# Optimization experiments

Measured on AMD Instinct MI355X. Metric: run time of the kernel, lower is better.

The kernel has to match this reference:

```python
import jax, jax.numpy as jnp
import numpy as np

# ---- quantization constants (8-bit, per-tensor affine; representative values) ----
Q_MAX = 255.0
S_IN, Z_IN = 0.05, 128.0      # block input
S1, Z1 = 0.04, 128.0          # after expand 1x1 + hardswish
S2, Z2 = 0.04, 128.0          # after depthwise 5x5 + hardswish
S_SE1, Z_SE1 = 0.03, 128.0    # SE fc1 output
S_SE2, Z_SE2 = 1.0 / 255.0, 0.0  # SE fc2 hardsigmoid output in [0,1]
S_MUL, Z_MUL = 0.04, 128.0    # SE gated activation
S3, Z3 = 0.05, 128.0          # after project 1x1
S_OUT, Z_OUT = 0.06, 128.0    # after residual add
W_SCALE = 0.01                # symmetric per-tensor weight scale (zero_point = 0)
EXP_C = 576                   # expanded channels (depthwise groups)


def conv(x, w, stride=1, padding=0, groups=1):
    return jax.lax.conv_general_dilated(
        x, w, (stride, stride), [(padding, padding), (padding, padding)],
        feature_group_count=groups, dimension_numbers=('NCHW', 'OIHW', 'NCHW'))


def hardswish(x):
    return x * jnp.clip(x + 3.0, 0.0, 6.0) * (1.0 / 6.0)


def hardsigmoid(x):
    return jnp.clip(x + 3.0, 0.0, 6.0) * (1.0 / 6.0)


def qconv(x_q, w_q, b_q, s_in, z_in, s_out, z_out, stride=1, padding=0, groups=1, act=None):
    """Quantized conv: int-domain accumulation (simulated in fp32), fused activation
    on the dequantized accumulator, then requantize to [0, Q_MAX]."""
    acc = conv(x_q - z_in, w_q, stride, padding, groups) + b_q[None, :, None, None]
    deq = acc * (s_in * W_SCALE)  # dequantize accumulator
    if act == 'hardswish':
        deq = hardswish(deq)
    elif act == 'hardsigmoid':
        deq = hardsigmoid(deq)
    return jnp.clip(deq * (1.0 / s_out) + z_out, 0.0, Q_MAX)


def setup_inputs() -> dict:
    key = jax.random.key(0)
    ks = jax.random.split(key, 11)
    def qw(k, shape):  # int8-style symmetric weights stored as fp32 integers
        return jnp.round(jnp.clip(jax.random.normal(k, shape) * 40.0, -127.0, 127.0))
    def qb(k, n):      # int32-style bias in accumulator domain
        return jnp.round(jax.random.normal(k, (n,)) * 500.0)
    return {
        'x':      jnp.round(jax.random.uniform(ks[0], (64, 96, 28, 28)) * Q_MAX),
        'w_exp':  qw(ks[1], (576, 96, 1, 1)),  'b_exp':  qb(ks[2], 576),
        'w_dw':   qw(ks[3], (576, 1, 5, 5)),   'b_dw':   qb(ks[4], 576),
        'w_se1':  qw(ks[5], (144, 576, 1, 1)), 'b_se1':  qb(ks[6], 144),
        'w_se2':  qw(ks[7], (576, 144, 1, 1)), 'b_se2':  qb(ks[8], 576),
        'w_proj': qw(ks[9], (96, 576, 1, 1)),  'b_proj': qb(ks[10], 96),
    }


def reference(x, w_exp, b_exp, w_dw, b_dw, w_se1, b_se1, w_se2, b_se2, w_proj, b_proj):
    # expand 1x1 (+ hardswish)
    e = qconv(x, w_exp, b_exp, S_IN, Z_IN, S1, Z1, act='hardswish')
    # depthwise 5x5, padding=(5-1)//2=2, groups=expanded (+ hardswish)
    d = qconv(e, w_dw, b_dw, S1, Z1, S2, Z2, padding=2, groups=EXP_C, act='hardswish')
    # squeeze-excitation: global avg pool -> fc1 -> fc2(hardsigmoid) -> quantized mul
    pooled = jnp.mean(d, axis=(2, 3), keepdims=True)  # [N, 576, 1, 1]
    g1 = qconv(pooled, w_se1, b_se1, S2, Z2, S_SE1, Z_SE1)
    g2 = qconv(g1, w_se2, b_se2, S_SE1, Z_SE1, S_SE2, Z_SE2, act='hardsigmoid')
    gated = jnp.clip((g2 - Z_SE2) * (d - Z2) * (S_SE2 * S2 / S_MUL) + Z_MUL, 0.0, Q_MAX)
    # project 1x1 (linear)
    p = qconv(gated, w_proj, b_proj, S_MUL, Z_MUL, S3, Z3)
    # quantized residual add (stride=1, in==out channels -> use_res_connect)
    out = jnp.clip((x - Z_IN) * (S_IN / S_OUT) + (p - Z3) * (S3 / S_OUT) + Z_OUT, 0.0, Q_MAX)
    return out
```

## Files before the change

kernel.cpp:

```cpp
#include <hip/hip_runtime.h>

typedef _Float16 v8h __attribute__((ext_vector_type(8)));
typedef _Float16 v4h __attribute__((ext_vector_type(4)));
typedef _Float16 v2h __attribute__((ext_vector_type(2)));
typedef float v4f __attribute__((ext_vector_type(4)));

#define NB 64
#define CI 96
#define CE 576
#define CO 96
#define HW 784
#define SEC 144

#if defined(__has_builtin)
#if __has_builtin(__builtin_amdgcn_fdot2)
#define HAVE_FDOT2 1
#endif
#endif

__device__ __forceinline__ float fdot2(v2h a, v2h b, float c) {
#ifdef HAVE_FDOT2
  return __builtin_amdgcn_fdot2(a, b, c, false);
#else
  return (float)a[0] * (float)b[0] + ((float)a[1] * (float)b[1] + c);
#endif
}

__global__ __launch_bounds__(256) void k0_cvt_w(const float* __restrict__ w_exp,
                                                const float* __restrict__ w_proj,
                                                _Float16* __restrict__ w_exp_h,
                                                _Float16* __restrict__ w_proj_h) {
  int i = blockIdx.x * 256 + threadIdx.x;
  if (i < CE * CI) {
    w_exp_h[i]  = (_Float16)w_exp[i];
    w_proj_h[i] = (_Float16)w_proj[i];
  }
}

__global__ __launch_bounds__(256) void k0x_pack(const float* __restrict__ x,
                                                _Float16* __restrict__ x_f) {
  __shared__ _Float16 xl[112][104];
  const int tid = threadIdx.x;
  const int n = blockIdx.y;
  const int hw0 = blockIdx.x * 112;

  for (int idx = tid; idx < CI * 28; idx += 256) {
    int c = idx / 28, seg = idx % 28;
    const float4 v = *(const float4*)&x[(n * CI + c) * HW + hw0 + seg * 4];
    int row = seg * 4;
    xl[row + 0][c] = (_Float16)(v.x - 128.0f);
    xl[row + 1][c] = (_Float16)(v.y - 128.0f);
    xl[row + 2][c] = (_Float16)(v.z - 128.0f);
    xl[row + 3][c] = (_Float16)(v.w - 128.0f);
  }
  __syncthreads();

  for (int idx = tid; idx < 1344; idx += 256) {
    int t_l = idx / 192, rem = idx % 192, s = rem / 64, ln = rem % 64;
    int hw_l = t_l * 16 + (ln & 15), ci = s * 32 + (ln >> 4) * 8;
    v8h o;
#pragma unroll
    for (int j = 0; j < 8; ++j) o[j] = xl[hw_l][ci + j];
    size_t t = (size_t)(blockIdx.x * 7 + t_l);
    *(v8h*)&x_f[(((size_t)n * 49 + t) * 3 + s) * 512 + ln * 8] = o;
  }
}

__global__ __launch_bounds__(512, 8) void k12_fused(const _Float16* __restrict__ x_f,
                                                    const _Float16* __restrict__ w_exp_h,
                                                    const float* __restrict__ b_exp,
                                                    const float* __restrict__ w_dw,
                                                    const float* __restrict__ b_dw,
                                                    _Float16* __restrict__ d_t,
                                                    float* __restrict__ d_sums2) {
  __shared__ _Float16 e_lds[16][18][38];
  __shared__ _Float16 d_tile[16][392];
  __shared__ _Float16 w_pairs[16][5][8];
  const int tid = threadIdx.x;
  const int n = blockIdx.z;
  const int h = blockIdx.y;
  const int c0 = blockIdx.x * 16;

  {
    unsigned long long* z = (unsigned long long*)&e_lds[0][0][0];
    for (int idx = tid; idx < 16 * 18 * 38 * 2 / 8; idx += 512) z[idx] = 0ull;
  }
  for (int idx = tid; idx < 640; idx += 512) {
    int c = idx / 40, r = idx % 40, dy = r / 8, k = r % 8;
    int tap = (k < 4) ? k : (k - 3);
    w_pairs[c][dy][k] = (_Float16)w_dw[(c0 + c) * 25 + dy * 5 + tap];
  }
  __syncthreads();

  const int wv = tid >> 6, lane = tid & 63;
  const int l15 = lane & 15, q = lane >> 4;

  {
    const _Float16* wrow = &w_exp_h[(c0 + l15) * CI + q * 8];
    v8h a0 = *(const v8h*)(wrow);
    v8h a1 = *(const v8h*)(wrow + 32);
    v8h a2 = *(const v8h*)(wrow + 64);
    float bia[4];
#pragma unroll
    for (int r = 0; r < 4; ++r) bia[r] = b_exp[c0 + q * 4 + r];

    const int ir0 = 14 * h - 2;
    const _Float16* xb = x_f + (size_t)n * (49 * 3 * 512) + lane * 8;
    for (int t_l = wv; t_l < 28; t_l += 8) {
      int t = 21 * h + t_l;
      const _Float16* xt = xb + (size_t)t * (3 * 512);
      v8h b0 = *(const v8h*)(xt);
      v8h b1 = *(const v8h*)(xt + 512);
      v8h b2 = *(const v8h*)(xt + 1024);
      v4f acc = (v4f){0.f, 0.f, 0.f, 0.f};
      acc = __builtin_amdgcn_mfma_f32_16x16x32_f16(a0, b0, acc, 0, 0, 0);
      acc = __builtin_amdgcn_mfma_f32_16x16x32_f16(a1, b1, acc, 0, 0, 0);
      acc = __builtin_amdgcn_mfma_f32_16x16x32_f16(a2, b2, acc, 0, 0, 0);
      int hw = t * 16 + l15;
      int y = hw / 28, xx = hw - y * 28;
      int r_l = y - ir0;
#pragma unroll
      for (int r = 0; r < 4; ++r) {
        float deq = (acc[r] + bia[r]) * 5.0e-4f;
        float cl  = fminf(fmaxf(deq + 3.0f, 0.0f), 6.0f);
        float ev  = fminf(fmaxf(deq * cl * (25.0f / 6.0f), -128.0f), 127.0f);
        e_lds[q * 4 + r][r_l][6 + xx] = (_Float16)ev;
      }
    }
  }
  __syncthreads();

  const int c = tid >> 5, l = tid & 31;
  v2h W01[5], W23[5], W12[5], W34[5];
  float W0s[5], W4s[5];
#pragma unroll
  for (int dy = 0; dy < 5; ++dy) {
    W01[dy] = *(const v2h*)&w_pairs[c][dy][0];
    W23[dy] = *(const v2h*)&w_pairs[c][dy][2];
    W12[dy] = *(const v2h*)&w_pairs[c][dy][4];
    W34[dy] = *(const v2h*)&w_pairs[c][dy][6];
    W0s[dy] = (float)W01[dy][0];
    W4s[dy] = (float)W34[dy][1];
  }
  const float bc = b_dw[c0 + c];

  float csum = 0.0f;
  if (l < 28) {
    const int ry = l >> 1;
    const int bx = (l & 1) * 14;
    v2h P0[5], P1[5], P2[5], P3[5];
#pragma unroll
    for (int dy = 0; dy < 5; ++dy) {
      const _Float16* row = &e_lds[c][ry + dy][bx];
      P0[dy] = *(const v2h*)(row + 4);
      P1[dy] = *(const v2h*)(row + 6);
      P2[dy] = *(const v2h*)(row + 8);
      P3[dy] = *(const v2h*)(row + 10);
    }
#pragma unroll
    for (int xi = 0; xi < 3; ++xi) {
      const int x0 = bx + xi * 4;
      float o0 = bc, o1 = bc, o2 = bc, o3 = bc;
#pragma unroll
      for (int dy = 0; dy < 5; ++dy) {
        o0 = fdot2(P0[dy], W01[dy], o0);
        o0 = fdot2(P1[dy], W23[dy], o0);
        o0 += (float)P2[dy][0] * W4s[dy];
        o1 += (float)P0[dy][1] * W0s[dy];
        o1 = fdot2(P1[dy], W12[dy], o1);
        o1 = fdot2(P2[dy], W34[dy], o1);
        o2 = fdot2(P1[dy], W01[dy], o2);
        o2 = fdot2(P2[dy], W23[dy], o2);
        o2 += (float)P3[dy][0] * W4s[dy];
        o3 += (float)P1[dy][1] * W0s[dy];
        o3 = fdot2(P2[dy], W12[dy], o3);
        o3 = fdot2(P3[dy], W34[dy], o3);
      }
      float oo[4] = {o0, o1, o2, o3};
      v2h dva, dvb;
#pragma unroll
      for (int i = 0; i < 4; ++i) {
        float deq = oo[i] * 4.0e-4f;
        float cl  = fminf(fmaxf(deq + 3.0f, 0.0f), 6.0f);
        float dvv = fminf(fmaxf(deq * cl * (25.0f / 6.0f), -128.0f), 127.0f);
        if (i < 2) dva[i] = (_Float16)dvv; else dvb[i - 2] = (_Float16)dvv;
        csum += dvv;
      }
      *(v2h*)&d_tile[c][ry * 28 + x0]     = dva;
      *(v2h*)&d_tile[c][ry * 28 + x0 + 2] = dvb;
#pragma unroll
      for (int dy = 0; dy < 5; ++dy) {
        const _Float16* row = &e_lds[c][ry + dy][bx];
        P0[dy] = P2[dy];
        P1[dy] = P3[dy];
        P2[dy] = *(const v2h*)(row + x0 - bx + 12);
        P3[dy] = *(const v2h*)(row + x0 - bx + 14);
      }
    }
    {
      float o0 = bc, o1 = bc;
#pragma unroll
      for (int dy = 0; dy < 5; ++dy) {
        o0 = fdot2(P0[dy], W01[dy], o0);
        o0 = fdot2(P1[dy], W23[dy], o0);
        o0 += (float)P2[dy][0] * W4s[dy];
        o1 += (float)P0[dy][1] * W0s[dy];
        o1 = fdot2(P1[dy], W12[dy], o1);
        o1 = fdot2(P2[dy], W34[dy], o1);
      }
      v2h dv;
      float oo[2] = {o0, o1};
#pragma unroll
      for (int i = 0; i < 2; ++i) {
        float deq = oo[i] * 4.0e-4f;
        float cl  = fminf(fmaxf(deq + 3.0f, 0.0f), 6.0f);
        float dvv = fminf(fmaxf(deq * cl * (25.0f / 6.0f), -128.0f), 127.0f);
        dv[i] = (_Float16)dvv;
        csum += dvv;
      }
      *(v2h*)&d_tile[c][ry * 28 + bx + 12] = dv;
    }
  }
#pragma unroll
  for (int m = 16; m >= 1; m >>= 1) csum += __shfl_xor(csum, m);
  if (l == 0) d_sums2[((size_t)h * NB + n) * CE + c0 + c] = csum;

  __syncthreads();
  const size_t obase = ((size_t)n * 72 + (c0 >> 3)) * 784 + 392 * h;
  if (tid < 392) {
    int hw_l = tid;
    v8h o0, o1;
#pragma unroll
    for (int j = 0; j < 8; ++j) { o0[j] = d_tile[j][hw_l]; o1[j] = d_tile[8 + j][hw_l]; }
    *(v8h*)&d_t[(obase + hw_l) * 8] = o0;
    *(v8h*)&d_t[(obase + 784 + hw_l) * 8] = o1;
  }
}

__global__ __launch_bounds__(256) void k3a_fc1(const float* __restrict__ d_sums2,
                                               const float* __restrict__ w_se1,
                                               const float* __restrict__ b_se1,
                                               float* __restrict__ g1) {
  const int tid = threadIdx.x;
  const int wv = tid >> 6, lane = tid & 63;
  const int n = blockIdx.y;
  const int o = blockIdx.x * 4 + wv;
  const float* wrow = &w_se1[o * CE];
  const float* s0 = &d_sums2[(size_t)n * CE];
  const float* s1 = &d_sums2[((size_t)NB + n) * CE];
  float p = 0.f;
#pragma unroll
  for (int s = 0; s < 9; ++s) {
    int cc = lane + s * 64;
    p += wrow[cc] * (s0[cc] + s1[cc]);
  }
#pragma unroll
  for (int m = 32; m >= 1; m >>= 1) p += __shfl_xor(p, m);
  if (lane == 0) {
    float deq = (p * (1.0f / 784.0f) + b_se1[o]) * 4.0e-4f;
    g1[n * SEC + o] = fminf(fmaxf(deq * 33.3333333f + 128.0f, 0.0f), 255.0f) - 128.0f;
  }
}

__global__ __launch_bounds__(256) void k3b_fc2(const float* __restrict__ g1,
                                               const float* __restrict__ w_se2,
                                               const float* __restrict__ b_se2,
                                               _Float16* __restrict__ g2h) {
  const int tid = threadIdx.x;
  const int wv = tid >> 6, lane = tid & 63;
  const int n = blockIdx.y;
  const int o = blockIdx.x * 4 + wv;
  const float* wrow = &w_se2[o * SEC];
  const float* grow = &g1[n * SEC];
  float p = wrow[lane] * grow[lane] + wrow[lane + 64] * grow[lane + 64];
  if (lane < 16) p += wrow[lane + 128] * grow[lane + 128];
#pragma unroll
  for (int m = 32; m >= 1; m >>= 1) p += __shfl_xor(p, m);
  if (lane == 0) {
    float deq = (p + b_se2[o]) * 3.0e-4f;
    g2h[n * CE + o] =
        (_Float16)(fminf(fmaxf(deq + 3.0f, 0.0f), 6.0f) * (1.0f / 6.0f));
  }
}

__global__ __launch_bounds__(192) void k4_proj(const _Float16* __restrict__ d_t,
                                               const _Float16* __restrict__ g2h,
                                               const _Float16* __restrict__ w_proj_h,
                                               const float* __restrict__ b_proj,
                                               const float* __restrict__ x,
                                               float* __restrict__ out) {
  const int tid = threadIdx.x;
  const int n = blockIdx.z;
  const int co0 = blockIdx.y * 48;
  const int hw0 = blockIdx.x * 112;
  const int wv = tid >> 6, lane = tid & 63;
  const int l15 = lane & 15, q = lane >> 4;

  v4f acc[7];
#pragma unroll
  for (int t = 0; t < 7; ++t) acc[t] = (v4f){0.f, 0.f, 0.f, 0.f};

  const _Float16* dbase = d_t + (((size_t)n * 72 + q) * 784 + hw0 + l15) * 8;
  const _Float16* abase = &w_proj_h[(co0 + wv * 16 + l15) * CE + q * 8];
  const _Float16* gbase = &g2h[(size_t)n * CE + q * 8];

  for (int ks = 0; ks < 18; ++ks) {
    v8h a = *(const v8h*)(abase + ks * 32);
    v8h g = *(const v8h*)(gbase + ks * 32);
    v8h ag = a * g;
    const _Float16* dk = dbase + (size_t)ks * (4 * 784 * 8);
#pragma unroll
    for (int t = 0; t < 7; ++t) {
      v8h b = *(const v8h*)(dk + t * (16 * 8));
      acc[t] = __builtin_amdgcn_mfma_f32_16x16x32_f16(ag, b, acc[t], 0, 0, 0);
    }
  }

  float bia[4];
#pragma unroll
  for (int r = 0; r < 4; ++r) bia[r] = b_proj[co0 + wv * 16 + q * 4 + r];

#pragma unroll
  for (int t = 0; t < 7; ++t) {
#pragma unroll
    for (int r = 0; r < 4; ++r) {
      int co = co0 + wv * 16 + q * 4 + r;
      int hw = hw0 + t * 16 + l15;
      float p = fminf(fmaxf((acc[t][r] + bia[r]) * 4.0e-4f * 20.0f + 128.0f, 0.0f), 255.0f);
      float xv = x[(n * CO + co) * HW + hw];
      float o = (xv - 128.0f) * 0.8333333333f + (p - 128.0f) * 0.8333333333f + 128.0f;
      out[(n * CO + co) * HW + hw] = fminf(fmaxf(o, 0.0f), 255.0f);
    }
  }
}

extern "C" void kernel_launch(void* const* d_in, const int* in_sizes, int n_in,
                              void* d_out, int out_size, void* d_ws, size_t ws_size,
                              hipStream_t stream) {
  const float* x      = (const float*)d_in[0];
  const float* w_exp  = (const float*)d_in[1];
  const float* b_exp  = (const float*)d_in[2];
  const float* w_dw   = (const float*)d_in[3];
  const float* b_dw   = (const float*)d_in[4];
  const float* w_se1  = (const float*)d_in[5];
  const float* b_se1  = (const float*)d_in[6];
  const float* w_se2  = (const float*)d_in[7];
  const float* b_se2  = (const float*)d_in[8];
  const float* w_proj = (const float*)d_in[9];
  const float* b_proj = (const float*)d_in[10];
  float* out = (float*)d_out;

  char* ws = (char*)d_ws;
  const size_t SZ_W  = (size_t)CE * CI * 2;
  const size_t SZ_XF = (size_t)NB * 49 * 3 * 512 * 2;
  const size_t SZ_D  = (size_t)NB * CE * HW * 2;
  const size_t SZ_S2 = (size_t)2 * NB * CE * 4;
  const size_t SZ_S  = (size_t)NB * CE * 4;
  _Float16* w_exp_h  = (_Float16*)(ws);
  _Float16* w_proj_h = (_Float16*)(ws + SZ_W);
  _Float16* x_f      = (_Float16*)(ws + 2 * SZ_W);
  _Float16* d_t      = (_Float16*)(ws + 2 * SZ_W + SZ_XF);
  float*    d_sums2  = (float*)   (ws + 2 * SZ_W + SZ_XF + SZ_D);
  float*    g1       = (float*)   (ws + 2 * SZ_W + SZ_XF + SZ_D + SZ_S2);
  _Float16* g2h      = (_Float16*)(ws + 2 * SZ_W + SZ_XF + SZ_D + SZ_S2 + SZ_S);

  k0_cvt_w<<<(CE * CI + 255) / 256, 256, 0, stream>>>(w_exp, w_proj, w_exp_h, w_proj_h);
  k0x_pack<<<dim3(7, NB), 256, 0, stream>>>(x, x_f);
  k12_fused<<<dim3(36, 2, NB), 512, 0, stream>>>(x_f, w_exp_h, b_exp, w_dw, b_dw, d_t, d_sums2);
  k3a_fc1<<<dim3(36, NB), 256, 0, stream>>>(d_sums2, w_se1, b_se1, g1);
  k3b_fc2<<<dim3(144, NB), 256, 0, stream>>>(g1, w_se2, b_se2, g2h);
  k4_proj<<<dim3(7, 2, NB), 192, 0, stream>>>(d_t, g2h, w_proj_h, b_proj, x, out);
}
```

Before: 175.6 us.

## Swap MFMA operand roles for vectorized LDS stores and repack depthwise weights

The expand GEMM now puts activations in the A operand and weights in B, so each lane holds four consecutive spatial outputs of one channel and writes them to LDS as a single 4-wide store instead of four scalar stores. The padded LDS row is widened and the halo offset shifted to keep those stores aligned. The depthwise weights are repacked as three pairs per row with a zero-padded fifth tap, and the odd-aligned outputs build shifted input pairs so every tap uses fdot2 instead of scalar fp32 multiplies. Launch bounds drop from 8 to 6 waves to allow more registers, at the cost of possibly lower occupancy and some extra permute work.

```diff
diff --git a/kernel.cpp b/kernel.cpp
--- a/kernel.cpp
+++ b/kernel.cpp
@@ -66,16 +66,16 @@
   }
 }
 
-__global__ __launch_bounds__(512, 8) void k12_fused(const _Float16* __restrict__ x_f,
+__global__ __launch_bounds__(512, 6) void k12_fused(const _Float16* __restrict__ x_f,
                                                     const _Float16* __restrict__ w_exp_h,
                                                     const float* __restrict__ b_exp,
                                                     const float* __restrict__ w_dw,
                                                     const float* __restrict__ b_dw,
                                                     _Float16* __restrict__ d_t,
                                                     float* __restrict__ d_sums2) {
-  __shared__ _Float16 e_lds[16][18][38];
+  __shared__ _Float16 e_lds[16][18][42];
   __shared__ _Float16 d_tile[16][392];
-  __shared__ _Float16 w_pairs[16][5][8];
+  __shared__ _Float16 w_pr[16][5][6];
   const int tid = threadIdx.x;
   const int n = blockIdx.z;
   const int h = blockIdx.y;
@@ -83,12 +83,11 @@
 
   {
     unsigned long long* z = (unsigned long long*)&e_lds[0][0][0];
-    for (int idx = tid; idx < 16 * 18 * 38 * 2 / 8; idx += 512) z[idx] = 0ull;
-  }
-  for (int idx = tid; idx < 640; idx += 512) {
-    int c = idx / 40, r = idx % 40, dy = r / 8, k = r % 8;
-    int tap = (k < 4) ? k : (k - 3);
-    w_pairs[c][dy][k] = (_Float16)w_dw[(c0 + c) * 25 + dy * 5 + tap];
+    for (int idx = tid; idx < 16 * 18 * 42 * 2 / 8; idx += 512) z[idx] = 0ull;
+  }
+  for (int idx = tid; idx < 480; idx += 512) {
+    int c = idx / 30, r = idx % 30, dy = r / 6, k = r % 6;
+    w_pr[c][dy][k] = (k < 5) ? (_Float16)w_dw[(c0 + c) * 25 + dy * 5 + k] : (_Float16)0.f;
   }
   __syncthreads();
 
@@ -97,50 +96,46 @@
 
   {
     const _Float16* wrow = &w_exp_h[(c0 + l15) * CI + q * 8];
-    v8h a0 = *(const v8h*)(wrow);
-    v8h a1 = *(const v8h*)(wrow + 32);
-    v8h a2 = *(const v8h*)(wrow + 64);
-    float bia[4];
-#pragma unroll
-    for (int r = 0; r < 4; ++r) bia[r] = b_exp[c0 + q * 4 + r];
+    v8h b0 = *(const v8h*)(wrow);
+    v8h b1 = *(const v8h*)(wrow + 32);
+    v8h b2 = *(const v8h*)(wrow + 64);
+    const float bia = b_exp[c0 + l15];
 
     const int ir0 = 14 * h - 2;
     const _Float16* xb = x_f + (size_t)n * (49 * 3 * 512) + lane * 8;
     for (int t_l = wv; t_l < 28; t_l += 8) {
       int t = 21 * h + t_l;
       const _Float16* xt = xb + (size_t)t * (3 * 512);
-      v8h b0 = *(const v8h*)(xt);
-      v8h b1 = *(const v8h*)(xt + 512);
-      v8h b2 = *(const v8h*)(xt + 1024);
+      v8h a0 = *(const v8h*)(xt);
+      v8h a1 = *(const v8h*)(xt + 512);
+      v8h a2 = *(const v8h*)(xt + 1024);
       v4f acc = (v4f){0.f, 0.f, 0.f, 0.f};
       acc = __builtin_amdgcn_mfma_f32_16x16x32_f16(a0, b0, acc, 0, 0, 0);
       acc = __builtin_amdgcn_mfma_f32_16x16x32_f16(a1, b1, acc, 0, 0, 0);
       acc = __builtin_amdgcn_mfma_f32_16x16x32_f16(a2, b2, acc, 0, 0, 0);
-      int hw = t * 16 + l15;
-      int y = hw / 28, xx = hw - y * 28;
+      int p = t * 16 + q * 4;
+      int y = p / 28, xx = p - y * 28;
       int r_l = y - ir0;
+      v4h ev;
 #pragma unroll
       for (int r = 0; r < 4; ++r) {
-        float deq = (acc[r] + bia[r]) * 5.0e-4f;
+        float deq = (acc[r] + bia) * 5.0e-4f;
         float cl  = fminf(fmaxf(deq + 3.0f, 0.0f), 6.0f);
-        float ev  = fminf(fmaxf(deq * cl * (25.0f / 6.0f), -128.0f), 127.0f);
-        e_lds[q * 4 + r][r_l][6 + xx] = (_Float16)ev;
-      }
+        float evf = fminf(fmaxf(deq * cl * (25.0f / 6.0f), -128.0f), 127.0f);
+        ev[r] = (_Float16)evf;
+      }
+      *(v4h*)&e_lds[l15][r_l][8 + xx] = ev;
     }
   }
   __syncthreads();
 
   const int c = tid >> 5, l = tid & 31;
-  v2h W01[5], W23[5], W12[5], W34[5];
-  float W0s[5], W4s[5];
+  v2h W01[5], W23[5], W40[5];
 #pragma unroll
   for (int dy = 0; dy < 5; ++dy) {
-    W01[dy] = *(const v2h*)&w_pairs[c][dy][0];
-    W23[dy] = *(const v2h*)&w_pairs[c][dy][2];
-    W12[dy] = *(const v2h*)&w_pairs[c][dy][4];
-    W34[dy] = *(const v2h*)&w_pairs[c][dy][6];
-    W0s[dy] = (float)W01[dy][0];
-    W4s[dy] = (float)W34[dy][1];
+    W01[dy] = *(const v2h*)&w_pr[c][dy][0];
+    W23[dy] = *(const v2h*)&w_pr[c][dy][2];
+    W40[dy] = *(const v2h*)&w_pr[c][dy][4];
   }
   const float bc = b_dw[c0 + c];
 
@@ -152,10 +147,10 @@
 #pragma unroll
     for (int dy = 0; dy < 5; ++dy) {
       const _Float16* row = &e_lds[c][ry + dy][bx];
-      P0[dy] = *(const v2h*)(row + 4);
-      P1[dy] = *(const v2h*)(row + 6);
-      P2[dy] = *(const v2h*)(row + 8);
-      P3[dy] = *(const v2h*)(row + 10);
+      P0[dy] = *(const v2h*)(row + 6);
+      P1[dy] = *(const v2h*)(row + 8);
+      P2[dy] = *(const v2h*)(row + 10);
+      P3[dy] = *(const v2h*)(row + 12);
     }
 #pragma unroll
     for (int xi = 0; xi < 3; ++xi) {
@@ -163,18 +158,14 @@
       float o0 = bc, o1 = bc, o2 = bc, o3 = bc;
 #pragma unroll
       for (int dy = 0; dy < 5; ++dy) {
-        o0 = fdot2(P0[dy], W01[dy], o0);
-        o0 = fdot2(P1[dy], W23[dy], o0);
-        o0 += (float)P2[dy][0] * W4s[dy];
-        o1 += (float)P0[dy][1] * W0s[dy];
-        o1 = fdot2(P1[dy], W12[dy], o1);
-        o1 = fdot2(P2[dy], W34[dy], o1);
-        o2 = fdot2(P1[dy], W01[dy], o2);
-        o2 = fdot2(P2[dy], W23[dy], o2);
-        o2 += (float)P3[dy][0] * W4s[dy];
-        o3 += (float)P1[dy][1] * W0s[dy];
-        o3 = fdot2(P2[dy], W12[dy], o3);
-        o3 = fdot2(P3[dy], W34[dy], o3);
+        v2h Q0 = (v2h){P0[dy][1], P1[dy][0]};
+        v2h Q1 = (v2h){P1[dy][1], P2[dy][0]};
+        v2h Q2 = (v2h){P2[dy][1], P3[dy][0]};
+        v2h Q3 = (v2h){P3[dy][1], (_Float16)0.f};
+        o0 = fdot2(P0[dy], W01[dy], fdot2(P1[dy], W23[dy], fdot2(P2[dy], W40[dy], o0)));
+        o1 = fdot2(Q0, W01[dy], fdot2(Q1, W23[dy], fdot2(Q2, W40[dy], o1)));
+        o2 = fdot2(P1[dy], W01[dy], fdot2(P2[dy], W23[dy], fdot2(P3[dy], W40[dy], o2)));
+        o3 = fdot2(Q1, W01[dy], fdot2(Q2, W23[dy], fdot2(Q3, W40[dy], o3)));
       }
       float oo[4] = {o0, o1, o2, o3};
       v2h dva, dvb;
@@ -193,20 +184,19 @@
         const _Float16* row = &e_lds[c][ry + dy][bx];
         P0[dy] = P2[dy];
         P1[dy] = P3[dy];
-        P2[dy] = *(const v2h*)(row + x0 - bx + 12);
-        P3[dy] = *(const v2h*)(row + x0 - bx + 14);
+        P2[dy] = *(const v2h*)(row + x0 - bx + 14);
+        P3[dy] = *(const v2h*)(row + x0 - bx + 16);
       }
     }
     {
       float o0 = bc, o1 = bc;
 #pragma unroll
       for (int dy = 0; dy < 5; ++dy) {
-        o0 = fdot2(P0[dy], W01[dy], o0);
-        o0 = fdot2(P1[dy], W23[dy], o0);
-        o0 += (float)P2[dy][0] * W4s[dy];
-        o1 += (float)P0[dy][1] * W0s[dy];
-        o1 = fdot2(P1[dy], W12[dy], o1);
-        o1 = fdot2(P2[dy], W34[dy], o1);
+        v2h Q0 = (v2h){P0[dy][1], P1[dy][0]};
+        v2h Q1 = (v2h){P1[dy][1], P2[dy][0]};
+        v2h Q2 = (v2h){P2[dy][1], P3[dy][0]};
+        o0 = fdot2(P0[dy], W01[dy], fdot2(P1[dy], W23[dy], fdot2(P2[dy], W40[dy], o0)));
+        o1 = fdot2(Q0, W01[dy], fdot2(Q1, W23[dy], fdot2(Q2, W40[dy], o1)));
       }
       v2h dv;
       float oo[2] = {o0, o1};
```

New measurement: 182.0 us. 3.6% more time.

## Fuse weight conversion into pack kernel, swap MFMA operands, read fp16 residual

Applied to the files above, without the earlier changes.

Folds the weight fp16 conversion into the x-pack kernel, which removes one launch. The expand MFMA now has its A/B operands swapped, so each lane gets four consecutive spatial outputs for one channel. Those are written as a single 4-wide LDS store into a re-padded e_lds tile, replacing four scalar stores. The pack kernel also writes an fp16 copy of the centered input, and the projection kernel reads that copy for the residual instead of the fp32 x, halving those bytes. The cost is an extra 9.6 MB fp16 write in the pack stage, and the residual now carries fp16 precision, which is exact for integer inputs.

```diff
diff --git a/kernel.cpp b/kernel.cpp
--- a/kernel.cpp
+++ b/kernel.cpp
@@ -26,32 +26,39 @@
 #endif
 }
 
-__global__ __launch_bounds__(256) void k0_cvt_w(const float* __restrict__ w_exp,
+__global__ __launch_bounds__(256) void k0x_pack(const float* __restrict__ x,
+                                                const float* __restrict__ w_exp,
                                                 const float* __restrict__ w_proj,
+                                                _Float16* __restrict__ x_f,
+                                                _Float16* __restrict__ x_h,
                                                 _Float16* __restrict__ w_exp_h,
                                                 _Float16* __restrict__ w_proj_h) {
-  int i = blockIdx.x * 256 + threadIdx.x;
-  if (i < CE * CI) {
-    w_exp_h[i]  = (_Float16)w_exp[i];
-    w_proj_h[i] = (_Float16)w_proj[i];
-  }
-}
-
-__global__ __launch_bounds__(256) void k0x_pack(const float* __restrict__ x,
-                                                _Float16* __restrict__ x_f) {
   __shared__ _Float16 xl[112][104];
   const int tid = threadIdx.x;
   const int n = blockIdx.y;
   const int hw0 = blockIdx.x * 112;
+
+  if (n == 0) {
+    for (int i = blockIdx.x * 256 + tid; i < CE * CI; i += 7 * 256) {
+      w_exp_h[i]  = (_Float16)w_exp[i];
+      w_proj_h[i] = (_Float16)w_proj[i];
+    }
+  }
 
   for (int idx = tid; idx < CI * 28; idx += 256) {
     int c = idx / 28, seg = idx % 28;
     const float4 v = *(const float4*)&x[(n * CI + c) * HW + hw0 + seg * 4];
     int row = seg * 4;
-    xl[row + 0][c] = (_Float16)(v.x - 128.0f);
-    xl[row + 1][c] = (_Float16)(v.y - 128.0f);
-    xl[row + 2][c] = (_Float16)(v.z - 128.0f);
-    xl[row + 3][c] = (_Float16)(v.w - 128.0f);
+    v4h xh;
+    xh[0] = (_Float16)(v.x - 128.0f);
+    xh[1] = (_Float16)(v.y - 128.0f);
+    xh[2] = (_Float16)(v.z - 128.0f);
+    xh[3] = (_Float16)(v.w - 128.0f);
+    xl[row + 0][c] = xh[0];
+    xl[row + 1][c] = xh[1];
+    xl[row + 2][c] = xh[2];
+    xl[row + 3][c] = xh[3];
+    *(v4h*)&x_h[(n * CI + c) * HW + hw0 + seg * 4] = xh;
   }
   __syncthreads();
 
@@ -73,7 +80,7 @@
                                                     const float* __restrict__ b_dw,
                                                     _Float16* __restrict__ d_t,
                                                     float* __restrict__ d_sums2) {
-  __shared__ _Float16 e_lds[16][18][38];
+  __shared__ _Float16 e_lds[16][18][42];
   __shared__ _Float16 d_tile[16][392];
   __shared__ _Float16 w_pairs[16][5][8];
   const int tid = threadIdx.x;
@@ -83,7 +90,7 @@
 
   {
     unsigned long long* z = (unsigned long long*)&e_lds[0][0][0];
-    for (int idx = tid; idx < 16 * 18 * 38 * 2 / 8; idx += 512) z[idx] = 0ull;
+    for (int idx = tid; idx < 16 * 18 * 42 * 2 / 8; idx += 512) z[idx] = 0ull;
   }
   for (int idx = tid; idx < 640; idx += 512) {
     int c = idx / 40, r = idx % 40, dy = r / 8, k = r % 8;
@@ -97,35 +104,35 @@
 
   {
     const _Float16* wrow = &w_exp_h[(c0 + l15) * CI + q * 8];
-    v8h a0 = *(const v8h*)(wrow);
-    v8h a1 = *(const v8h*)(wrow + 32);
-    v8h a2 = *(const v8h*)(wrow + 64);
-    float bia[4];
-#pragma unroll
-    for (int r = 0; r < 4; ++r) bia[r] = b_exp[c0 + q * 4 + r];
+    v8h b0 = *(const v8h*)(wrow);
+    v8h b1 = *(const v8h*)(wrow + 32);
+    v8h b2 = *(const v8h*)(wrow + 64);
+    const float bia = b_exp[c0 + l15];
 
     const int ir0 = 14 * h - 2;
     const _Float16* xb = x_f + (size_t)n * (49 * 3 * 512) + lane * 8;
     for (int t_l = wv; t_l < 28; t_l += 8) {
       int t = 21 * h + t_l;
       const _Float16* xt = xb + (size_t)t * (3 * 512);
-      v8h b0 = *(const v8h*)(xt);
-      v8h b1 = *(const v8h*)(xt + 512);
-      v8h b2 = *(const v8h*)(xt + 1024);
+      v8h a0 = *(const v8h*)(xt);
+      v8h a1 = *(const v8h*)(xt + 512);
+      v8h a2 = *(const v8h*)(xt + 1024);
       v4f acc = (v4f){0.f, 0.f, 0.f, 0.f};
       acc = __builtin_amdgcn_mfma_f32_16x16x32_f16(a0, b0, acc, 0, 0, 0);
       acc = __builtin_amdgcn_mfma_f32_16x16x32_f16(a1, b1, acc, 0, 0, 0);
       acc = __builtin_amdgcn_mfma_f32_16x16x32_f16(a2, b2, acc, 0, 0, 0);
-      int hw = t * 16 + l15;
-      int y = hw / 28, xx = hw - y * 28;
+      int p = t * 16 + q * 4;
+      int y = p / 28, xx = p - y * 28;
       int r_l = y - ir0;
+      v4h ev;
 #pragma unroll
       for (int r = 0; r < 4; ++r) {
-        float deq = (acc[r] + bia[r]) * 5.0e-4f;
+        float deq = (acc[r] + bia) * 5.0e-4f;
         float cl  = fminf(fmaxf(deq + 3.0f, 0.0f), 6.0f);
-        float ev  = fminf(fmaxf(deq * cl * (25.0f / 6.0f), -128.0f), 127.0f);
-        e_lds[q * 4 + r][r_l][6 + xx] = (_Float16)ev;
-      }
+        float evf = fminf(fmaxf(deq * cl * (25.0f / 6.0f), -128.0f), 127.0f);
+        ev[r] = (_Float16)evf;
+      }
+      *(v4h*)&e_lds[l15][r_l][8 + xx] = ev;
     }
   }
   __syncthreads();
@@ -152,10 +159,10 @@
 #pragma unroll
     for (int dy = 0; dy < 5; ++dy) {
       const _Float16* row = &e_lds[c][ry + dy][bx];
-      P0[dy] = *(const v2h*)(row + 4);
-      P1[dy] = *(const v2h*)(row + 6);
-      P2[dy] = *(const v2h*)(row + 8);
-      P3[dy] = *(const v2h*)(row + 10);
+      P0[dy] = *(const v2h*)(row + 6);
+      P1[dy] = *(const v2h*)(row + 8);
+      P2[dy] = *(const v2h*)(row + 10);
+      P3[dy] = *(const v2h*)(row + 12);
     }
 #pragma unroll
     for (int xi = 0; xi < 3; ++xi) {
@@ -193,8 +200,8 @@
         const _Float16* row = &e_lds[c][ry + dy][bx];
         P0[dy] = P2[dy];
         P1[dy] = P3[dy];
-        P2[dy] = *(const v2h*)(row + x0 - bx + 12);
-        P3[dy] = *(const v2h*)(row + x0 - bx + 14);
+        P2[dy] = *(const v2h*)(row + x0 - bx + 14);
+        P3[dy] = *(const v2h*)(row + x0 - bx + 16);
       }
     }
     {
@@ -287,7 +294,7 @@
                                                const _Float16* __restrict__ g2h,
                                                const _Float16* __restrict__ w_proj_h,
                                                const float* __restrict__ b_proj,
-                                               const float* __restrict__ x,
+                                               const _Float16* __restrict__ x_h,
                                                float* __restrict__ out) {
   const int tid = threadIdx.x;
   const int n = blockIdx.z;
@@ -327,8 +334,8 @@
       int co = co0 + wv * 16 + q * 4 + r;
       int hw = hw0 + t * 16 + l15;
       float p = fminf(fmaxf((acc[t][r] + bia[r]) * 4.0e-4f * 20.0f + 128.0f, 0.0f), 255.0f);
-      float xv = x[(n * CO + co) * HW + hw];
-      float o = (xv - 128.0f) * 0.8333333333f + (p - 128.0f) * 0.8333333333f + 128.0f;
+      float xv = (float)x_h[(n * CO + co) * HW + hw];
+      float o = xv * 0.8333333333f + (p - 128.0f) * 0.8333333333f + 128.0f;
       out[(n * CO + co) * HW + hw] = fminf(fmaxf(o, 0.0f), 255.0f);
     }
   }
@@ -353,21 +360,22 @@
   char* ws = (char*)d_ws;
   const size_t SZ_W  = (size_t)CE * CI * 2;
   const size_t SZ_XF = (size_t)NB * 49 * 3 * 512 * 2;
+  const size_t SZ_XH = (size_t)NB * CI * HW * 2;
   const size_t SZ_D  = (size_t)NB * CE * HW * 2;
   const size_t SZ_S2 = (size_t)2 * NB * CE * 4;
   const size_t SZ_S  = (size_t)NB * CE * 4;
   _Float16* w_exp_h  = (_Float16*)(ws);
   _Float16* w_proj_h = (_Float16*)(ws + SZ_W);
   _Float16* x_f      = (_Float16*)(ws + 2 * SZ_W);
-  _Float16* d_t      = (_Float16*)(ws + 2 * SZ_W + SZ_XF);
-  float*    d_sums2  = (float*)   (ws + 2 * SZ_W + SZ_XF + SZ_D);
-  float*    g1       = (float*)   (ws + 2 * SZ_W + SZ_XF + SZ_D + SZ_S2);
-  _Float16* g2h      = (_Float16*)(ws + 2 * SZ_W + SZ_XF + SZ_D + SZ_S2 + SZ_S);
-
-  k0_cvt_w<<<(CE * CI + 255) / 256, 256, 0, stream>>>(w_exp, w_proj, w_exp_h, w_proj_h);
-  k0x_pack<<<dim3(7, NB), 256, 0, stream>>>(x, x_f);
+  _Float16* x_h      = (_Float16*)(ws + 2 * SZ_W + SZ_XF);
+  _Float16* d_t      = (_Float16*)(ws + 2 * SZ_W + SZ_XF + SZ_XH);
+  float*    d_sums2  = (float*)   (ws + 2 * SZ_W + SZ_XF + SZ_XH + SZ_D);
+  float*    g1       = (float*)   (ws + 2 * SZ_W + SZ_XF + SZ_XH + SZ_D + SZ_S2);
+  _Float16* g2h      = (_Float16*)(ws + 2 * SZ_W + SZ_XF + SZ_XH + SZ_D + SZ_S2 + SZ_S);
+
+  k0x_pack<<<dim3(7, NB), 256, 0, stream>>>(x, w_exp, w_proj, x_f, x_h, w_exp_h, w_proj_h);
   k12_fused<<<dim3(36, 2, NB), 512, 0, stream>>>(x_f, w_exp_h, b_exp, w_dw, b_dw, d_t, d_sums2);
   k3a_fc1<<<dim3(36, NB), 256, 0, stream>>>(d_sums2, w_se1, b_se1, g1);
   k3b_fc2<<<dim3(144, NB), 256, 0, stream>>>(g1, w_se2, b_se2, g2h);
-  k4_proj<<<dim3(7, 2, NB), 192, 0, stream>>>(d_t, g2h, w_proj_h, b_proj, x, out);
-}
+  k4_proj<<<dim3(7, 2, NB), 192, 0, stream>>>(d_t, g2h, w_proj_h, b_proj, x_h, out);
+}
```

After: 177.7 us. Within noise of the previous version (+1.2%).
